# Performance work log

Measured on AMD Instinct MI355X. Metric: run time of the kernel, lower is better.

Reference implementation:

```python
import jax, jax.numpy as jnp
import numpy as np

B, N, H, F = 4, 4096, 128, 64
ADJ_DENSITY = 0.01


def setup_inputs() -> dict:
    key = jax.random.key(0)
    k1, k2, k3, k4, k5 = jax.random.split(key, 5)
    x = jax.random.normal(k1, (B, N, H), dtype=jnp.float32)
    w_scale = jnp.float32(1.0 / np.sqrt(H))  # ~ nn.Linear init scale
    Wq = jax.random.normal(k2, (H, F), dtype=jnp.float32) * w_scale
    Wk = jax.random.normal(k3, (H, F), dtype=jnp.float32) * w_scale
    Wv = jax.random.normal(k4, (H, F), dtype=jnp.float32) * w_scale
    # Sparse binary adjacency with self-loops (every row has >=1 neighbor,
    # so no all--inf softmax rows).
    adj = (jax.random.uniform(k5, (N, N)) < ADJ_DENSITY).astype(jnp.float32)
    diag = jnp.arange(N)
    adj = adj.at[diag, diag].set(1.0)
    return {"x": x, "Wq": Wq, "Wk": Wk, "Wv": Wv, "adj": adj}


def reference(x, Wq, Wk, Wv, adj):
    # x: (B,N,H); Wq/Wk/Wv: (H,F); adj: (N,N) binary, broadcast over batch.
    q = x @ Wq  # (B,N,F)
    k = x @ Wk  # (B,N,F)
    v = x @ Wv  # (B,N,F)
    scale = jnp.float32(F) ** -0.5  # k.shape[-1] ** -0.5
    scores = jnp.einsum("bnf,bmf->bnm", q, k) * scale  # (B,N,N)
    scores = jnp.where(adj[None] == 0, -jnp.inf, scores)
    # softmax over neighbors, then the module adds the adjacency back (wei + adj)
    wei = jax.nn.softmax(scores, axis=-1) + adj[None]  # (B,N,N)
    # dropout is identity in eval/deterministic reference
    out = jnp.einsum("bnm,bmf->bnf", wei, v)  # (B,N,F)
    return out
```

## Files before the change

kernel.cpp:

```cpp
#include <hip/hip_runtime.h>
#include <math.h>

#define Bb 4
#define Nn 4096
#define Hh 128
#define Ff 64
#define CAP 128

typedef __attribute__((ext_vector_type(8))) short bf16x8;
typedef __attribute__((ext_vector_type(4))) float f32x4;

__device__ __forceinline__ unsigned short f2bf(float f) {
  unsigned int u = __float_as_uint(f);
  u += 0x7fffu + ((u >> 16) & 1u);
  return (unsigned short)(u >> 16);
}
__device__ __forceinline__ float bf2f(unsigned short h) {
  return __uint_as_float(((unsigned int)h) << 16);
}

__global__ __launch_bounds__(256) void prep_kernel(
    const float* __restrict__ x,
    const float* __restrict__ Wq,
    const float* __restrict__ Wk,
    const float* __restrict__ Wv,
    const float* __restrict__ adj,
    float* __restrict__ q,
    unsigned short* __restrict__ kb,
    unsigned short* __restrict__ vb,
    unsigned short* __restrict__ g_nbr, int* __restrict__ g_cnt) {
  __shared__ short xs[64 * 128];
  __shared__ __align__(8) unsigned short stg[4][CAP];

  const int tid = threadIdx.x;
  const int w = tid >> 6;
  const int lane = tid & 63;
  const int bid = (int)blockIdx.x;

  if ((bid % 5) == 4) {
    const int row0 = (bid / 5) * 64;
    const int half = lane >> 4;
    const int l16 = lane & 15;

    const float4* xg = (const float4*)(x + (size_t)row0 * Hh);
#pragma unroll
    for (int j = 0; j < 8; ++j) {
      const int idx = tid + 256 * j;
      const int row = idx >> 5;
      const int c4 = idx & 31;
      const float4 xv = xg[idx];
      uint2 p;
      p.x = (unsigned)f2bf(xv.x) | ((unsigned)f2bf(xv.y) << 16);
      p.y = (unsigned)f2bf(xv.z) | ((unsigned)f2bf(xv.w) << 16);
      const int addr = (row * 256 + c4 * 8) ^ ((row & 7) << 4);
      *(uint2*)((char*)xs + addr) = p;
    }

    bf16x8 bfr[3][4];
#pragma unroll
    for (int nt = 0; nt < 3; ++nt) {
      const int n0g = w * 48 + nt * 16;
      const float* Wm = (n0g < 64) ? Wq : (n0g < 128) ? Wk : Wv;
      const int c0 = n0g & 63;
#pragma unroll
      for (int ks = 0; ks < 4; ++ks) {
        bf16x8 f;
#pragma unroll
        for (int j = 0; j < 8; ++j) {
          const int kr = ks * 32 + half * 8 + j;
          f[j] = (short)f2bf(Wm[kr * Ff + c0 + l16]);
        }
        bfr[nt][ks] = f;
      }
    }
    __syncthreads();

    f32x4 acc[4][3];
#pragma unroll
    for (int mt = 0; mt < 4; ++mt)
#pragma unroll
      for (int nt = 0; nt < 3; ++nt)
#pragma unroll
        for (int r = 0; r < 4; ++r) acc[mt][nt][r] = 0.f;

#pragma unroll
    for (int mt = 0; mt < 4; ++mt) {
      const int arow = mt * 16 + l16;
      const int abase = arow * 256;
      const int aswz = (arow & 7) << 4;
#pragma unroll
      for (int ks = 0; ks < 4; ++ks) {
        const int addr = (abase + ks * 64 + half * 16) ^ aswz;
        const bf16x8 a = *(const bf16x8*)((const char*)xs + addr);
#pragma unroll
        for (int nt = 0; nt < 3; ++nt) {
          acc[mt][nt] = __builtin_amdgcn_mfma_f32_16x16x32_bf16(
              a, bfr[nt][ks], acc[mt][nt], 0, 0, 0);
        }
      }
    }

#pragma unroll
    for (int mt = 0; mt < 4; ++mt) {
#pragma unroll
      for (int nt = 0; nt < 3; ++nt) {
        const int n0g = w * 48 + nt * 16;
        const int col = (n0g & 63) + l16;
#pragma unroll
        for (int r = 0; r < 4; ++r) {
          const size_t rowg = (size_t)row0 + mt * 16 + half * 4 + r;
          const float val = acc[mt][nt][r];
          if (n0g < 64)
            q[rowg * Ff + col] = val;
          else if (n0g < 128)
            kb[rowg * Ff + col] = f2bf(val);
          else
            vb[rowg * Ff + col] = f2bf(val);
        }
      }
    }
  } else {
    const int csr_idx = (bid / 5) * 4 + (bid % 5);
    const int n = csr_idx * 4 + w;
    const float4* ap = (const float4*)(adj + (size_t)n * Nn);
    unsigned short* srow = stg[w];

    ((ushort2*)srow)[lane] = make_ushort2(0, 0);

    float4 a4[16];
#pragma unroll
    for (int j = 0; j < 16; ++j) a4[j] = ap[j * 64 + lane];

    int cnt = 0;
#pragma unroll
    for (int j = 0; j < 16; ++j) {
      cnt += (a4[j].x != 0.f) + (a4[j].y != 0.f) + (a4[j].z != 0.f) +
             (a4[j].w != 0.f);
    }

    int inc = cnt;
#pragma unroll
    for (int o = 1; o < 64; o <<= 1) {
      const int t = __shfl_up(inc, o, 64);
      if (lane >= o) inc += t;
    }

    int pos = inc - cnt;
#pragma unroll
    for (int j = 0; j < 16; ++j) {
      const int col0 = 4 * (j * 64 + lane);
#pragma unroll
      for (int comp = 0; comp < 4; ++comp) {
        const float val = comp == 0 ? a4[j].x
                        : comp == 1 ? a4[j].y
                        : comp == 2 ? a4[j].z
                                    : a4[j].w;
        if (val != 0.f) {
          if (pos < CAP) srow[pos] = (unsigned short)(col0 + comp);
          ++pos;
        }
      }
    }

    const int tot = __shfl(inc, 63, 64);
    if (lane == 0) g_cnt[n] = tot < CAP ? tot : CAP;
    ((ushort2*)(g_nbr + (size_t)n * CAP))[lane] = ((const ushort2*)srow)[lane];
  }
}

__global__ __launch_bounds__(256) void attn_kernel(
    const unsigned short* __restrict__ g_nbr,
    const int* __restrict__ g_cnt,
    const float* __restrict__ q,
    const unsigned short* __restrict__ kb,
    const unsigned short* __restrict__ vb,
    float* __restrict__ out) {
  __shared__ __align__(8) unsigned short nbr[CAP];
  __shared__ float qs[4][64];
  __shared__ float ps[4][64];

  const int n = blockIdx.x;
  const int tid = threadIdx.x;
  const int w = tid >> 6;
  const int lane = tid & 63;

  qs[w][lane] = q[((size_t)w * Nn + n) * Ff + lane];
  if (w == 0) {
    ((ushort2*)nbr)[lane] = ((const ushort2*)(g_nbr + (size_t)n * CAP))[lane];
  }
  const int tot = g_cnt[n];
  __syncthreads();

  const int b = w;
  const unsigned short* kbb = kb + (size_t)b * Nn * Ff;
  const unsigned short* vbb = vb + (size_t)b * Nn * Ff;

  const int g = lane >> 2;
  const int sl = lane & 3;

  float4 q0a = *(const float4*)&qs[b][8 * sl];
  float4 q0b = *(const float4*)&qs[b][8 * sl + 4];
  float4 q1a = *(const float4*)&qs[b][32 + 8 * sl];
  float4 q1b = *(const float4*)&qs[b][32 + 8 * sl + 4];

  float M = -INFINITY, L = 0.f, acc = 0.f, vsum = 0.f;

  const int ntiles = (tot + 63) >> 6;
  for (int t = 0; t < ntiles; ++t) {
    const int tbase = t << 6;

    float s0, s1, s2, s3;
#define BPAIR(u, qlo, qhi, a)                                   \
    {                                                           \
      const float flo = __uint_as_float((u) << 16);             \
      const float fhi = __uint_as_float((u) & 0xffff0000u);     \
      a = fmaf(qlo, flo, a);                                    \
      a = fmaf(qhi, fhi, a);                                    \
    }
#define DOT_ROW(i, sdst)                                                  \
    {                                                                     \
      const int idx = tbase + g + 16 * (i);                               \
      const bool valid = idx < tot;                                       \
      const int m = valid ? (int)nbr[idx] : 0;                            \
      const char* krow = (const char*)(kbb + (size_t)m * Ff);             \
      const uint4 k0 = *(const uint4*)(krow + 16 * sl);                   \
      const uint4 k1 = *(const uint4*)(krow + 64 + 16 * sl);              \
      float a = 0.f;                                                      \
      BPAIR(k0.x, q0a.x, q0a.y, a)                                        \
      BPAIR(k0.y, q0a.z, q0a.w, a)                                        \
      BPAIR(k0.z, q0b.x, q0b.y, a)                                        \
      BPAIR(k0.w, q0b.z, q0b.w, a)                                        \
      BPAIR(k1.x, q1a.x, q1a.y, a)                                        \
      BPAIR(k1.y, q1a.z, q1a.w, a)                                        \
      BPAIR(k1.z, q1b.x, q1b.y, a)                                        \
      BPAIR(k1.w, q1b.z, q1b.w, a)                                        \
      a += __shfl_xor(a, 1, 64);                                          \
      a += __shfl_xor(a, 2, 64);                                          \
      sdst = valid ? a * 0.125f : -INFINITY;                              \
    }
    DOT_ROW(0, s0)
    DOT_ROW(1, s1)
    DOT_ROW(2, s2)
    DOT_ROW(3, s3)
#undef DOT_ROW
#undef BPAIR

    float lm = fmaxf(fmaxf(s0, s1), fmaxf(s2, s3));
#pragma unroll
    for (int o = 32; o; o >>= 1) lm = fmaxf(lm, __shfl_xor(lm, o, 64));
    const float newM = fmaxf(M, lm);

    const float p0 = (s0 == -INFINITY) ? 0.f : __expf(s0 - newM);
    const float p1 = (s1 == -INFINITY) ? 0.f : __expf(s1 - newM);
    const float p2 = (s2 == -INFINITY) ? 0.f : __expf(s2 - newM);
    const float p3 = (s3 == -INFINITY) ? 0.f : __expf(s3 - newM);

    float psum = ((p0 + p1) + (p2 + p3));
#pragma unroll
    for (int o = 32; o >= 4; o >>= 1) psum += __shfl_xor(psum, o, 64);

    const float corr = __expf(M - newM);
    L = L * corr + psum;
    acc *= corr;
    M = newM;

    const float pw = sl == 0 ? p0 : sl == 1 ? p1 : sl == 2 ? p2 : p3;
    ps[w][g + 16 * sl] = pw;

    const int jmax = min(64, tot - tbase);
#pragma unroll 4
    for (int j = 0; j < jmax; ++j) {
      const int m = nbr[tbase + j];
      const float vf = bf2f(vbb[(size_t)m * Ff + lane]);
      acc = fmaf(ps[w][j], vf, acc);
      vsum += vf;
    }
  }

  out[((size_t)b * Nn + n) * Ff + lane] = acc / L + vsum;
}

extern "C" void kernel_launch(void* const* d_in, const int* in_sizes, int n_in,
                              void* d_out, int out_size, void* d_ws, size_t ws_size,
                              hipStream_t stream) {
  const float* x = (const float*)d_in[0];
  const float* Wq = (const float*)d_in[1];
  const float* Wk = (const float*)d_in[2];
  const float* Wv = (const float*)d_in[3];
  const float* adj = (const float*)d_in[4];
  float* out = (float*)d_out;

  char* ws = (char*)d_ws;
  const size_t rows = (size_t)Bb * Nn;
  float* q = (float*)ws;
  unsigned short* kb = (unsigned short*)(ws + rows * Ff * 4);
  unsigned short* vb = (unsigned short*)(ws + rows * Ff * 4 + rows * Ff * 2);
  unsigned short* g_nbr = (unsigned short*)(ws + rows * Ff * 8);
  int* g_cnt = (int*)(ws + rows * Ff * 8 + (size_t)Nn * CAP * 2);

  prep_kernel<<<dim3(1280), dim3(256), 0, stream>>>(
      x, Wq, Wk, Wv, adj, q, kb, vb, g_nbr, g_cnt);
  attn_kernel<<<dim3(Nn), dim3(256), 0, stream>>>(g_nbr, g_cnt, q, kb, vb, out);
}
```

Measured before the change: 48.51 us.

## Replace CSR neighbor build with ballot bitmask, expand in attention kernel

The prep kernel no longer builds per-row compacted neighbor lists with a prefix scan. It now scans the adjacency matrix with wave ballots and writes a 4096-bit mask per row. The attention kernel reads the 64 words of its row's mask, prefix-sums their popcounts and expands the set bits into the neighbor list in shared memory. This aims to cut the per-row scan and scatter work in prep and spread the adjacency read over more blocks. In exchange it adds a serial bit-expansion loop and a scan at the start of each attention block.

New measurement: 47.38 us. 1.02x faster.

```diff
diff --git a/kernel.cpp b/kernel.cpp
--- a/kernel.cpp
+++ b/kernel.cpp
@@ -19,7 +19,7 @@
   return __uint_as_float(((unsigned int)h) << 16);
 }
 
-__global__ __launch_bounds__(256) void prep_kernel(
+__global__ __launch_bounds__(256) void prep2_kernel(
     const float* __restrict__ x,
     const float* __restrict__ Wq,
     const float* __restrict__ Wk,
@@ -28,17 +28,16 @@
     float* __restrict__ q,
     unsigned short* __restrict__ kb,
     unsigned short* __restrict__ vb,
-    unsigned short* __restrict__ g_nbr, int* __restrict__ g_cnt) {
+    unsigned long long* __restrict__ bm) {
   __shared__ short xs[64 * 128];
-  __shared__ __align__(8) unsigned short stg[4][CAP];
 
   const int tid = threadIdx.x;
   const int w = tid >> 6;
   const int lane = tid & 63;
   const int bid = (int)blockIdx.x;
 
-  if ((bid % 5) == 4) {
-    const int row0 = (bid / 5) * 64;
+  if (bid < 256) {
+    const int row0 = bid * 64;
     const int half = lane >> 4;
     const int l16 = lane & 15;
 
@@ -120,57 +119,29 @@
       }
     }
   } else {
-    const int csr_idx = (bid / 5) * 4 + (bid % 5);
-    const int n = csr_idx * 4 + w;
-    const float4* ap = (const float4*)(adj + (size_t)n * Nn);
-    unsigned short* srow = stg[w];
-
-    ((ushort2*)srow)[lane] = make_ushort2(0, 0);
-
-    float4 a4[16];
-#pragma unroll
-    for (int j = 0; j < 16; ++j) a4[j] = ap[j * 64 + lane];
-
-    int cnt = 0;
-#pragma unroll
-    for (int j = 0; j < 16; ++j) {
-      cnt += (a4[j].x != 0.f) + (a4[j].y != 0.f) + (a4[j].z != 0.f) +
-             (a4[j].w != 0.f);
-    }
-
-    int inc = cnt;
-#pragma unroll
-    for (int o = 1; o < 64; o <<= 1) {
-      const int t = __shfl_up(inc, o, 64);
-      if (lane >= o) inc += t;
-    }
-
-    int pos = inc - cnt;
-#pragma unroll
-    for (int j = 0; j < 16; ++j) {
-      const int col0 = 4 * (j * 64 + lane);
-#pragma unroll
-      for (int comp = 0; comp < 4; ++comp) {
-        const float val = comp == 0 ? a4[j].x
-                        : comp == 1 ? a4[j].y
-                        : comp == 2 ? a4[j].z
-                                    : a4[j].w;
-        if (val != 0.f) {
-          if (pos < CAP) srow[pos] = (unsigned short)(col0 + comp);
-          ++pos;
-        }
-      }
-    }
-
-    const int tot = __shfl(inc, 63, 64);
-    if (lane == 0) g_cnt[n] = tot < CAP ? tot : CAP;
-    ((ushort2*)(g_nbr + (size_t)n * CAP))[lane] = ((const ushort2*)srow)[lane];
+    const int sid = bid - 256;
+    const int wg = sid * 4 + w;
+    const float4* base = ((const float4*)adj) + ((size_t)wg * 8) * 64 + lane;
+
+    float4 a[8];
+#pragma unroll
+    for (int it = 0; it < 8; ++it) a[it] = base[it * 64];
+
+#pragma unroll
+    for (int it = 0; it < 8; ++it) {
+      const unsigned long long b0 = __ballot(a[it].x != 0.f);
+      const unsigned long long b1 = __ballot(a[it].y != 0.f);
+      const unsigned long long b2 = __ballot(a[it].z != 0.f);
+      const unsigned long long b3 = __ballot(a[it].w != 0.f);
+      const unsigned long long bsel =
+          lane == 0 ? b0 : lane == 1 ? b1 : lane == 2 ? b2 : b3;
+      if (lane < 4) bm[((size_t)wg * 8 + it) * 4 + lane] = bsel;
+    }
   }
 }
 
 __global__ __launch_bounds__(256) void attn_kernel(
-    const unsigned short* __restrict__ g_nbr,
-    const int* __restrict__ g_cnt,
+    const unsigned long long* __restrict__ bm,
     const float* __restrict__ q,
     const unsigned short* __restrict__ kb,
     const unsigned short* __restrict__ vb,
@@ -178,6 +149,7 @@
   __shared__ __align__(8) unsigned short nbr[CAP];
   __shared__ float qs[4][64];
   __shared__ float ps[4][64];
+  __shared__ int s_tot;
 
   const int n = blockIdx.x;
   const int tid = threadIdx.x;
@@ -185,11 +157,29 @@
   const int lane = tid & 63;
 
   qs[w][lane] = q[((size_t)w * Nn + n) * Ff + lane];
+
   if (w == 0) {
-    ((ushort2*)nbr)[lane] = ((const ushort2*)(g_nbr + (size_t)n * CAP))[lane];
+    unsigned long long m = bm[(size_t)n * 64 + lane];
+    const int cnt = __popcll(m);
+    int inc = cnt;
+#pragma unroll
+    for (int o = 1; o < 64; o <<= 1) {
+      const int t = __shfl_up(inc, o, 64);
+      if (lane >= o) inc += t;
+    }
+    int pos = inc - cnt;
+    const int colbase = ((lane >> 2) << 8) + (lane & 3);
+    while (m) {
+      const int i = __builtin_ctzll(m);
+      if (pos < CAP) nbr[pos] = (unsigned short)(colbase + (i << 2));
+      ++pos;
+      m &= m - 1;
+    }
+    if (lane == 63) s_tot = inc;
   }
-  const int tot = g_cnt[n];
   __syncthreads();
+
+  const int tot = s_tot < CAP ? s_tot : CAP;
 
   const int b = w;
   const unsigned short* kbb = kb + (size_t)b * Nn * Ff;
@@ -295,10 +285,9 @@
   float* q = (float*)ws;
   unsigned short* kb = (unsigned short*)(ws + rows * Ff * 4);
   unsigned short* vb = (unsigned short*)(ws + rows * Ff * 4 + rows * Ff * 2);
-  unsigned short* g_nbr = (unsigned short*)(ws + rows * Ff * 8);
-  int* g_cnt = (int*)(ws + rows * Ff * 8 + (size_t)Nn * CAP * 2);
-
-  prep_kernel<<<dim3(1280), dim3(256), 0, stream>>>(
-      x, Wq, Wk, Wv, adj, q, kb, vb, g_nbr, g_cnt);
-  attn_kernel<<<dim3(Nn), dim3(256), 0, stream>>>(g_nbr, g_cnt, q, kb, vb, out);
-}
+  unsigned long long* bm = (unsigned long long*)(ws + rows * Ff * 8);
+
+  prep2_kernel<<<dim3(2304), dim3(256), 0, stream>>>(
+      x, Wq, Wk, Wv, adj, q, kb, vb, bm);
+  attn_kernel<<<dim3(Nn), dim3(256), 0, stream>>>(bm, q, kb, vb, out);
+}
```
